# Optimization experiments

Hardware: AMD Instinct MI355X
Metric: run time of the kernel (lower is better)

The kernel has to match this reference:

```python
import jax, jax.numpy as jnp
import numpy as np
from jax import lax

B = 32
ITERS = 100
ALPHA = 0.3  # keras LeakyReLU default alpha
BN_SCALE = np.float32(1.0 / np.sqrt(1.0 + 1e-3))  # inference BN, default moving stats (mean 0, var 1)


def _make_psf_mat():
    # Gaussian PSF mapping 5184 fine (72x72) code positions -> 81 coarse (9x9) pixels, mat shape (5184, 81)
    sigma = (150.0 / 100.0) * 9.0 / 64.0
    coarse = np.arange(9) + 0.5
    fine = (np.arange(72) + 0.5) * 9.0 / 72.0
    g = np.exp(-(fine[:, None] - coarse[None, :]) ** 2 / (2.0 * sigma ** 2))  # (72, 9)
    mat = np.einsum('ia,jb->ijab', g, g).reshape(5184, 81)
    mat = mat / np.linalg.norm(mat, ord=2)  # spectral-normalize so FISTA (mu=1) is stable
    return mat.astype(np.float32)


def leaky(x):
    return jnp.where(x >= 0, x, ALPHA * x)


def conv(x, k, strides=(1, 1)):
    return lax.conv_general_dilated(x, k, strides, 'SAME',
                                    dimension_numbers=('NHWC', 'HWIO', 'NHWC'))


def _forward(inp, mat, w1_k, w1_b, x1_k, x1_b, c51_k, c51_b, c15_k, c15_b,
             c55_k, c55_b, x2_k, x2_b, y17_k, y17_b, y71_k, y71_b, yc_k, yc_b,
             d1_k, d2_k, h1_w, h1_b, h2_w, h2_b, h3_w, h3_b):
    b = inp.shape[0]
    # w branch
    w = leaky(conv(inp, w1_k) + w1_b)  # (B,9,9,1)
    # z branch -> lambda parameter
    z = inp * BN_SCALE
    z = leaky(conv(z, d1_k, strides=(3, 3)) * BN_SCALE)  # (B,3,3,12), downsample: conv no-bias + BN + LeakyReLU
    z = leaky(conv(z, d2_k, strides=(3, 3)) * BN_SCALE)  # (B,1,1,24)
    z = z.reshape(b, -1)
    z = z @ h1_w + h1_b
    z = z @ h2_w + h2_b
    z = z @ h3_w + h3_b  # (B,1)
    param = 0.1 * jax.nn.sigmoid(z)  # (B,1)
    # x branch: normalize (max of |x| over axis 1 only, as in source)
    x = inp / (0.001 + jnp.max(jnp.abs(inp), axis=1, keepdims=True))
    x = leaky(conv(x, x1_k) + x1_b)  # (B,9,9,3)
    # --- CompressedSensing: 100-iter FISTA, vectorized over batch and 3 channels ---
    im = x.reshape(b, 81, 3).transpose(0, 2, 1)  # (B,3,81) row-major flatten per channel
    lam = (param * 0.1)[:, :, None]  # (B,1,1), mu = 1.0

    def step(carry, _):
        y_tmp, y_last, t = carry
        resid = im - jnp.einsum('bcn,nk->bck', y_tmp, mat)      # (B,3,81)  = im - mat^T y
        re = jnp.einsum('bck,nk->bcn', resid, mat)              # (B,3,5184) = mat (im - mat^T y)
        wv = y_tmp + re
        y_new = jax.nn.relu(wv - lam) - jax.nn.relu(-wv - lam)  # soft threshold
        t_n = (1.0 + jnp.sqrt(1.0 + 4.0 * t * t)) / 2.0
        y_next = y_new + (t - 1.0) / t_n * (y_new - y_last)
        return (y_next, y_new, t_n), None

    init = (jnp.zeros((b, 3, 5184), jnp.float32),
            jnp.zeros((b, 3, 5184), jnp.float32),
            jnp.float32(1.0))
    (_, y_new, _), _ = lax.scan(step, init, None, length=ITERS)
    cs_out = y_new.transpose(0, 2, 1).reshape(b, 72, 72, 3)  # stack channels last then reshape
    x = conv(cs_out, c51_k, strides=(2, 2)) + c51_b   # (B,36,36,16), no activation
    x = conv(x, c15_k, strides=(2, 2)) + c15_b        # (B,18,18,32)
    x = conv(x, c55_k, strides=(2, 2)) + c55_b        # (B,9,9,64)
    x = leaky(conv(x, x2_k) + x2_b)                   # (B,9,9,8)
    # y branch
    y1 = conv(inp, y17_k) + y17_b                     # (B,9,9,32)
    y2 = conv(inp, y71_k) + y71_b                     # (B,9,9,32)
    y = leaky(conv(jnp.concatenate([y1, y2], axis=-1), yc_k) + yc_b)  # (B,9,9,32)
    out = jnp.concatenate([w, x, y], axis=-1)         # (B,9,9,41)
    return out, cs_out


def setup_inputs() -> dict:
    key = jax.random.key(0)
    ks = jax.random.split(key, 20)
    rn = lambda k, s, sc=0.1: sc * jax.random.normal(k, s, dtype=jnp.float32)
    x1_k = jnp.clip(1.0 + 0.3 * jax.random.normal(ks[1], (1, 1, 3, 3)), 0.0, None).astype(jnp.float32)
    return {
        'inp': jax.random.normal(ks[0], (B, 9, 9, 3), dtype=jnp.float32),
        'mat': jnp.asarray(_make_psf_mat()),
        'w1_k': rn(ks[2], (1, 1, 3, 1)), 'w1_b': jnp.zeros((1,), jnp.float32),
        'x1_k': x1_k, 'x1_b': jnp.zeros((3,), jnp.float32),
        'c51_k': rn(ks[3], (5, 1, 3, 16)), 'c51_b': jnp.zeros((16,), jnp.float32),
        'c15_k': rn(ks[4], (1, 5, 16, 32)), 'c15_b': jnp.zeros((32,), jnp.float32),
        'c55_k': rn(ks[5], (5, 5, 32, 64)), 'c55_b': jnp.zeros((64,), jnp.float32),
        'x2_k': rn(ks[6], (1, 1, 64, 8)), 'x2_b': jnp.zeros((8,), jnp.float32),
        'y17_k': rn(ks[7], (1, 7, 3, 32)), 'y17_b': jnp.zeros((32,), jnp.float32),
        'y71_k': rn(ks[8], (7, 1, 3, 32)), 'y71_b': jnp.zeros((32,), jnp.float32),
        'yc_k': rn(ks[9], (1, 1, 64, 32)), 'yc_b': jnp.zeros((32,), jnp.float32),
        'd1_k': rn(ks[10], (5, 5, 3, 12)), 'd2_k': rn(ks[11], (5, 5, 12, 24)),
        'h1_w': rn(ks[12], (24, 24), 0.2), 'h1_b': jnp.zeros((24,), jnp.float32),
        'h2_w': rn(ks[13], (24, 12), 0.2), 'h2_b': jnp.zeros((12,), jnp.float32),
        'h3_w': rn(ks[14], (12, 1), 0.2), 'h3_b': jnp.zeros((1,), jnp.float32),
    }


def reference(inp, mat, w1_k, w1_b, x1_k, x1_b, c51_k, c51_b, c15_k, c15_b,
              c55_k, c55_b, x2_k, x2_b, y17_k, y17_b, y71_k, y71_b, yc_k, yc_b,
              d1_k, d2_k, h1_w, h1_b, h2_w, h2_b, h3_w, h3_b):
    return _forward(inp, mat, w1_k, w1_b, x1_k, x1_b, c51_k, c51_b, c15_k, c15_b,
                    c55_k, c55_b, x2_k, x2_b, y17_k, y17_b, y71_k, y71_b, yc_k, yc_b,
                    d1_k, d2_k, h1_w, h1_b, h2_w, h2_b, h3_w, h3_b)
```

## Files before the change

### kernel.cpp

```cpp
#include <hip/hip_runtime.h>
#include <math.h>

#define LEAKY(x) ((x) >= 0.f ? (x) : 0.3f*(x))

#define G_OFF   0
#define IM_OFF  648
#define LAM_OFF 8424
#define WB_OFF  8456
#define YBR_OFF 11048
#define X2_OFF  757544

#define OUT0 106272

__global__ __launch_bounds__(256) void prep_kernel(
    const float* __restrict__ inp, const float* __restrict__ mat,
    const float* __restrict__ w1_k, const float* __restrict__ w1_b,
    const float* __restrict__ x1_k, const float* __restrict__ x1_b,
    const float* __restrict__ y17_k, const float* __restrict__ y17_b,
    const float* __restrict__ y71_k, const float* __restrict__ y71_b,
    const float* __restrict__ yc_k, const float* __restrict__ yc_b,
    const float* __restrict__ d1_k, const float* __restrict__ d2_k,
    const float* __restrict__ h1_w, const float* __restrict__ h1_b,
    const float* __restrict__ h2_w, const float* __restrict__ h2_b,
    const float* __restrict__ h3_w, const float* __restrict__ h3_b,
    float* __restrict__ ws)
{
    int t = threadIdx.x;
    if (blockIdx.x == 0) {
        float rs = rsqrtf(mat[0]);
        for (int u = t; u < 648; u += 256) {
            int i = u / 9, a = u % 9;
            ws[G_OFF + u] = mat[(size_t)(i*72)*81 + a*9] * rs;
        }
        return;
    }
    int b = blockIdx.x - 1;
    __shared__ float sin_[243];
    __shared__ float cm[27];
    __shared__ float cat[5184];
    __shared__ float z1[108];
    __shared__ float z2[24];
    __shared__ float v1[24];
    __shared__ float v2[12];

    const float BN  = 1.0f / sqrtf(1.001f);
    const float BN2 = BN * BN;

    for (int u = t; u < 243; u += 256) sin_[u] = inp[b*243 + u];
    __syncthreads();

    if (t < 81) {
        float s = w1_b[0];
        for (int i = 0; i < 3; ++i) s += sin_[t*3+i] * w1_k[i];
        ws[WB_OFF + b*81 + t] = LEAKY(s);
    } else if (t < 108) {
        int u = t - 81;
        float m = 0.f;
        for (int r = 0; r < 9; ++r) m = fmaxf(m, fabsf(sin_[r*27 + u]));
        cm[u] = 0.001f + m;
    }
    if (t >= 128 && t < 236) {
        int u = t - 128;
        int o = u % 12, ox = (u/12) % 3, oy = u/36;
        float s = 0.f;
        for (int kh = 0; kh < 5; ++kh) {
            int iy = oy*3 - 1 + kh;
            if (iy < 0 || iy > 8) continue;
            for (int kw = 0; kw < 5; ++kw) {
                int ix = ox*3 - 1 + kw;
                if (ix < 0 || ix > 8) continue;
                for (int i = 0; i < 3; ++i)
                    s += sin_[(iy*9+ix)*3 + i] * d1_k[((kh*5+kw)*3 + i)*12 + o];
            }
        }
        z1[u] = LEAKY(BN2 * s);
    }
    __syncthreads();

    if (t < 243) {
        int o = t / 81, p = t % 81;
        int c = p % 9;
        float s = x1_b[o];
        for (int i = 0; i < 3; ++i)
            s += (sin_[p*3+i] / cm[c*3+i]) * x1_k[i*3 + o];
        ws[IM_OFF + (b*3 + o)*81 + p] = LEAKY(s);
    }
    __syncthreads();

    if (t < 24) {
        float s = 0.f;
        for (int kh = 1; kh < 4; ++kh)
            for (int kw = 1; kw < 4; ++kw)
                for (int i = 0; i < 12; ++i)
                    s += z1[((kh-1)*3 + (kw-1))*12 + i] * d2_k[((kh*5+kw)*12 + i)*24 + t];
        z2[t] = LEAKY(BN * s);
    }
    __syncthreads();
    if (t < 24) {
        float s = h1_b[t];
        for (int i = 0; i < 24; ++i) s += z2[i] * h1_w[i*24 + t];
        v1[t] = s;
    }
    __syncthreads();
    if (t < 12) {
        float s = h2_b[t];
        for (int i = 0; i < 24; ++i) s += v1[i] * h2_w[i*12 + t];
        v2[t] = s;
    }
    __syncthreads();
    if (t == 0) {
        float s = h3_b[0];
        for (int i = 0; i < 12; ++i) s += v2[i] * h3_w[i];
        ws[LAM_OFF + b] = 0.01f / (1.f + expf(-s));
    }

    for (int u = t; u < 5184; u += 256) {
        int pos = u / 64, i = u % 64;
        int r = pos / 9, c = pos % 9;
        float s;
        if (i < 32) {
            s = y17_b[i];
            for (int kw = 0; kw < 7; ++kw) {
                int cc = c - 3 + kw;
                if (cc < 0 || cc > 8) continue;
                for (int ii = 0; ii < 3; ++ii)
                    s += sin_[(r*9+cc)*3 + ii] * y17_k[(kw*3+ii)*32 + i];
            }
        } else {
            int i2 = i - 32;
            s = y71_b[i2];
            for (int kh = 0; kh < 7; ++kh) {
                int rr = r - 3 + kh;
                if (rr < 0 || rr > 8) continue;
                for (int ii = 0; ii < 3; ++ii)
                    s += sin_[(rr*9+c)*3 + ii] * y71_k[(kh*3+ii)*32 + i2];
            }
        }
        cat[pos*64 + i] = s;
    }
    __syncthreads();
    for (int u = t; u < 2592; u += 256) {
        int pos = u / 32, o = u % 32;
        float s = yc_b[o];
        for (int i = 0; i < 64; ++i) s += cat[pos*64 + i] * yc_k[i*32 + o];
        ws[YBR_OFF + (b*81 + pos)*32 + o] = LEAKY(s);
    }
}


#define DPP_XOR1 0xB1
#define DPP_XOR2 0x4E
#define DPP_HM   0x141
#define DPP_ROR8 0x128

template<int CTRL>
__device__ __forceinline__ float dppadd(float v) {
    return v + __int_as_float(__builtin_amdgcn_update_dpp(
        0, __float_as_int(v), CTRL, 0xF, 0xF, true));
}

#define STEPMID(s,sm,sp) { \
    float re = gm*q##sm + g0*q##s + gp*q##sp; \
    float wv = Yv##s + re; \
    float cl = fminf(fmaxf(wv, -lam), lam); \
    float yn = wv - cl; \
    float yx = yn + cmom*(yn - Yl##s); \
    Yl##s = yn; Yv##s = yx; \
    u##sm += yx*gm; u##s += yx*g0; u##sp += yx*gp; }
#define STEP0 { \
    float re = g0*q0 + gp*q1; \
    float wv = Yv0 + re; \
    float cl = fminf(fmaxf(wv, -lam), lam); \
    float yn = wv - cl; \
    float yx = yn + cmom*(yn - Yl0); \
    Yl0 = yn; Yv0 = yx; \
    u0 += yx*g0; u1 += yx*gp; }
#define STEP8 { \
    float re = gm*q7 + g0*q8; \
    float wv = Yv8 + re; \
    float cl = fminf(fmaxf(wv, -lam), lam); \
    float yn = wv - cl; \
    float yx = yn + cmom*(yn - Yl8); \
    Yl8 = yn; Yv8 = yx; \
    u7 += yx*gm; u8 += yx*g0; }

#define TSP(a) { float v = u##a; \
    v = dppadd<DPP_XOR1>(v); v = dppadd<DPP_XOR2>(v); v = dppadd<DPP_HM>(v); \
    float vA = v*Gjg, vB = v*Gj8; \
    spA_##a = dppadd<DPP_ROR8>(vA); spB_##a = dppadd<DPP_ROR8>(vB); }

#define QT3(a) float q##a = cmc*rm_##a + c0c*r0_##a + cpc*rp_##a;

#define OUTW(s) cs_out[(size_t)(b*5184 + (8*s+gg)*72 + j)*3 + ch] = Yl##s;

__global__ __launch_bounds__(576, 3) void fista_kernel(
    const float* __restrict__ ws, float* __restrict__ cs_out)
{
    __shared__ __align__(16) float SPm[36*108];
    __shared__ __align__(16) float Rm[108];

    int t = threadIdx.x;
    int b = blockIdx.x / 3, ch = blockIdx.x % 3;
    const float* g = ws + G_OFF;
    float lam = ws[LAM_OFF + b];

    int j = t >> 3, gg = t & 7;
    int l = t & 63;
    int w = t >> 6;
    int rr = j & 7;

    float gm = g[(gg + 8)*9 + 0];
    float g0 = g[gg*9 + 0];
    float gp = g[gg*9 + 1];

    float cmc = (w > 0) ? g[(rr + 8)*9 + 0] : 0.f;
    float c0c = g[rr*9 + 0];
    float cpc = (w < 8) ? g[rr*9 + 1] : 0.f;
    int bmr = (w > 0) ? w - 1 : 0;
    int bpr = (w < 8) ? w + 1 : 8;

    float Gjg = g[j*9 + gg];
    float Gj8 = g[j*9 + 8];

    int ab = t >> 2, pp = t & 3;
    int aa = ab / 9, bb = ab % 9;
    float im_ab = (t < 324) ? ws[IM_OFF + (b*3 + ch)*81 + ab] : 0.f;

    if (t < 81) {
        Rm[(t % 9)*12 + (t / 9)] = ws[IM_OFF + (b*3 + ch)*81 + t];
    }

    float Yv0=0,Yv1=0,Yv2=0,Yv3=0,Yv4=0,Yv5=0,Yv6=0,Yv7=0,Yv8=0;
    float Yl0=0,Yl1=0,Yl2=0,Yl3=0,Yl4=0,Yl5=0,Yl6=0,Yl7=0,Yl8=0;
    float tk = 1.f;
    __syncthreads();

    for (int it = 0; it < 100; ++it) {
        float tn = 0.5f*(1.f + sqrtf(1.f + 4.f*tk*tk));
        float cmom = (tk - 1.f) / tn;
        tk = tn;

        float4 mv0 = *(const float4*)(Rm + bmr*12);
        float4 mv1 = *(const float4*)(Rm + bmr*12 + 4);
        float  mv2 = Rm[bmr*12 + 8];
        float rm_0=mv0.x, rm_1=mv0.y, rm_2=mv0.z, rm_3=mv0.w,
              rm_4=mv1.x, rm_5=mv1.y, rm_6=mv1.z, rm_7=mv1.w, rm_8=mv2;
        float4 zv0 = *(const float4*)(Rm + w*12);
        float4 zv1 = *(const float4*)(Rm + w*12 + 4);
        float  zv2 = Rm[w*12 + 8];
        float r0_0=zv0.x, r0_1=zv0.y, r0_2=zv0.z, r0_3=zv0.w,
              r0_4=zv1.x, r0_5=zv1.y, r0_6=zv1.z, r0_7=zv1.w, r0_8=zv2;
        float4 pv0 = *(const float4*)(Rm + bpr*12);
        float4 pv1 = *(const float4*)(Rm + bpr*12 + 4);
        float  pv2 = Rm[bpr*12 + 8];
        float rp_0=pv0.x, rp_1=pv0.y, rp_2=pv0.z, rp_3=pv0.w,
              rp_4=pv1.x, rp_5=pv1.y, rp_6=pv1.z, rp_7=pv1.w, rp_8=pv2;
        QT3(0) QT3(1) QT3(2) QT3(3) QT3(4) QT3(5) QT3(6) QT3(7) QT3(8)

        float u0=0,u1=0,u2=0,u3=0,u4=0,u5=0,u6=0,u7=0,u8=0;
        STEP0
        STEPMID(1,0,2) STEPMID(2,1,3) STEPMID(3,2,4) STEPMID(4,3,5)
        STEPMID(5,4,6) STEPMID(6,5,7) STEPMID(7,6,8)
        STEP8
        if (it == 99) break;

        float spA_0,spA_1,spA_2,spA_3,spA_4,spA_5,spA_6,spA_7,spA_8;
        float spB_0,spB_1,spB_2,spB_3,spB_4,spB_5,spB_6,spB_7,spB_8;
        TSP(0) TSP(1) TSP(2) TSP(3) TSP(4) TSP(5) TSP(6) TSP(7) TSP(8)

        int setb = ((t >> 6)*4 + (l >> 4))*108;
        if ((l & 8) == 0) {
            float* d = &SPm[setb + gg*12];
            ((float4*)d)[0] = make_float4(spA_0,spA_1,spA_2,spA_3);
            ((float4*)d)[1] = make_float4(spA_4,spA_5,spA_6,spA_7);
            d[8] = spA_8;
            if (gg == 0) {
                float* d2 = &SPm[setb + 96];
                ((float4*)d2)[0] = make_float4(spB_0,spB_1,spB_2,spB_3);
                ((float4*)d2)[1] = make_float4(spB_4,spB_5,spB_6,spB_7);
                d2[8] = spB_8;
            }
        }
        __syncthreads();

        if (t < 324) {
            float s = SPm[(bb*4 + pp)*108 + bb*12 + aa];
            if (bb > 0) s += SPm[((bb-1)*4 + pp)*108 + bb*12 + aa];
            if (bb < 8) s += SPm[((bb+1)*4 + pp)*108 + bb*12 + aa];
            s = dppadd<DPP_XOR1>(s);
            s = dppadd<DPP_XOR2>(s);
            if (pp == 0) Rm[bb*12 + aa] = im_ab - s;
        }
        __syncthreads();
    }

    OUTW(0) OUTW(1) OUTW(2) OUTW(3) OUTW(4) OUTW(5) OUTW(6) OUTW(7) OUTW(8)
}

__global__ __launch_bounds__(256) void c51c15_kernel(
    const float* __restrict__ cs, const float* __restrict__ k51,
    const float* __restrict__ b51, const float* __restrict__ k15,
    const float* __restrict__ b15, float* __restrict__ x2out)
{
    __shared__ float x1s[36*16];
    int t = threadIdx.x;
    int b = blockIdx.x / 18, oy = blockIdx.x % 18;

    for (int u = t; u < 36*16; u += 256) {
        int o = u & 15, ox = u >> 4;
        float s = b51[o];
        int ix = ox*2;
        for (int kh = 0; kh < 5; ++kh) {
            int iy = oy*4 - 1 + kh;
            if (iy < 0 || iy >= 72) continue;
            const float* p = cs + ((size_t)(b*72 + iy)*72 + ix)*3;
            const float* kk = k51 + kh*48 + o;
            s += p[0]*kk[0] + p[1]*kk[16] + p[2]*kk[32];
        }
        x1s[u] = s;
    }
    __syncthreads();

    for (int u = t; u < 18*32; u += 256) {
        int o = u & 31, ox = u >> 5;
        float s = b15[o];
        for (int kw = 0; kw < 5; ++kw) {
            int ix = ox*2 - 1 + kw;
            if (ix < 0 || ix >= 36) continue;
            const float* p = x1s + ix*16;
            const float* kk = k15 + kw*512 + o;
            for (int i = 0; i < 16; ++i) s += p[i]*kk[i*32];
        }
        x2out[((size_t)(b*18 + oy)*18 + ox)*32 + o] = s;
    }
}

__global__ __launch_bounds__(256) void c55out_kernel(
    const float* __restrict__ x2g, const float* __restrict__ k55,
    const float* __restrict__ b55, const float* __restrict__ ws,
    const float* __restrict__ x2_k, const float* __restrict__ x2_b,
    float* __restrict__ out)
{
    __shared__ float x3s[4][64];
    int t = threadIdx.x;
    int lp = t >> 6;
    int o  = t & 63;
    int pg = blockIdx.x*4 + lp;
    int b  = pg / 81, rc = pg % 81;
    int r  = rc / 9,  c  = rc % 9;

    {
        float s = b55[o];
        for (int kh = 0; kh < 5; ++kh) {
            int iy = r*2 - 1 + kh;
            if (iy < 0 || iy >= 18) continue;
            for (int kw = 0; kw < 5; ++kw) {
                int ix = c*2 - 1 + kw;
                if (ix < 0 || ix >= 18) continue;
                const float* p = x2g + ((size_t)(b*18 + iy)*18 + ix)*32;
                const float* kk = k55 + (kh*5+kw)*2048 + o;
                for (int i = 0; i < 32; ++i) s += p[i]*kk[i*64];
            }
        }
        x3s[lp][o] = s;
    }
    __syncthreads();

    if (t < 4*41) {
        int lp2 = t / 41, q = t % 41;
        int pg2 = blockIdx.x*4 + lp2;
        int b2  = pg2 / 81, rc2 = pg2 % 81;
        float val;
        if (q == 0) {
            val = ws[WB_OFF + b2*81 + rc2];
        } else if (q <= 8) {
            int o2 = q - 1;
            float s = x2_b[o2];
            for (int i = 0; i < 64; ++i) s += x3s[lp2][i]*x2_k[i*8 + o2];
            val = LEAKY(s);
        } else {
            val = ws[YBR_OFF + (size_t)(b2*81 + rc2)*32 + (q - 9)];
        }
        out[(size_t)pg2*41 + q] = val;
    }
}

extern "C" void kernel_launch(void* const* d_in, const int* in_sizes, int n_in,
                              void* d_out, int out_size, void* d_ws, size_t ws_size,
                              hipStream_t stream) {
    const float* inp   = (const float*)d_in[0];
    const float* mat   = (const float*)d_in[1];
    const float* w1_k  = (const float*)d_in[2];
    const float* w1_b  = (const float*)d_in[3];
    const float* x1_k  = (const float*)d_in[4];
    const float* x1_b  = (const float*)d_in[5];
    const float* c51_k = (const float*)d_in[6];
    const float* c51_b = (const float*)d_in[7];
    const float* c15_k = (const float*)d_in[8];
    const float* c15_b = (const float*)d_in[9];
    const float* c55_k = (const float*)d_in[10];
    const float* c55_b = (const float*)d_in[11];
    const float* x2_k  = (const float*)d_in[12];
    const float* x2_b  = (const float*)d_in[13];
    const float* y17_k = (const float*)d_in[14];
    const float* y17_b = (const float*)d_in[15];
    const float* y71_k = (const float*)d_in[16];
    const float* y71_b = (const float*)d_in[17];
    const float* yc_k  = (const float*)d_in[18];
    const float* yc_b  = (const float*)d_in[19];
    const float* d1_k  = (const float*)d_in[20];
    const float* d2_k  = (const float*)d_in[21];
    const float* h1_w  = (const float*)d_in[22];
    const float* h1_b  = (const float*)d_in[23];
    const float* h2_w  = (const float*)d_in[24];
    const float* h2_b  = (const float*)d_in[25];
    const float* h3_w  = (const float*)d_in[26];
    const float* h3_b  = (const float*)d_in[27];

    float* ws  = (float*)d_ws;
    float* out = (float*)d_out;
    float* cs  = out + OUT0;

    hipLaunchKernelGGL(prep_kernel, dim3(33), dim3(256), 0, stream,
        inp, mat, w1_k, w1_b, x1_k, x1_b, y17_k, y17_b, y71_k, y71_b,
        yc_k, yc_b, d1_k, d2_k, h1_w, h1_b, h2_w, h2_b, h3_w, h3_b, ws);
    hipLaunchKernelGGL(fista_kernel, dim3(96), dim3(576), 0, stream, ws, cs);
    hipLaunchKernelGGL(c51c15_kernel, dim3(576), dim3(256), 0, stream,
        cs, c51_k, c51_b, c15_k, c15_b, ws + X2_OFF);
    hipLaunchKernelGGL(c55out_kernel, dim3(648), dim3(256), 0, stream,
        ws + X2_OFF, c55_k, c55_b, ws, x2_k, x2_b, out);
}
```

Before: 346.7 us.

## Double-buffer partial sums and give each wavefront a private residual copy

```diff
diff --git a/kernel.cpp b/kernel.cpp
--- a/kernel.cpp
+++ b/kernel.cpp
@@ -152,6 +152,8 @@
 #define DPP_XOR2 0x4E
 #define DPP_HM   0x141
 #define DPP_ROR8 0x128
+
+#define SPHALF 3888
 
 template<int CTRL>
 __device__ __forceinline__ float dppadd(float v) {
@@ -196,8 +198,8 @@
 __global__ __launch_bounds__(576, 3) void fista_kernel(
     const float* __restrict__ ws, float* __restrict__ cs_out)
 {
-    __shared__ __align__(16) float SPm[36*108];
-    __shared__ __align__(16) float Rm[108];
+    __shared__ __align__(16) float SPm[2*SPHALF];
+    __shared__ __align__(16) float Rpriv[9*36];
 
     int t = threadIdx.x;
     int b = blockIdx.x / 3, ch = blockIdx.x % 3;
@@ -216,43 +218,48 @@
     float cmc = (w > 0) ? g[(rr + 8)*9 + 0] : 0.f;
     float c0c = g[rr*9 + 0];
     float cpc = (w < 8) ? g[rr*9 + 1] : 0.f;
-    int bmr = (w > 0) ? w - 1 : 0;
-    int bpr = (w < 8) ? w + 1 : 8;
 
     float Gjg = g[j*9 + gg];
     float Gj8 = g[j*9 + 8];
 
-    int ab = t >> 2, pp = t & 3;
-    int aa = ab / 9, bb = ab % 9;
-    float im_ab = (t < 324) ? ws[IM_OFF + (b*3 + ch)*81 + ab] : 0.f;
-
-    if (t < 81) {
-        Rm[(t % 9)*12 + (t / 9)] = ws[IM_OFF + (b*3 + ch)*81 + t];
-    }
+    int r3 = l / 18, rrem = l % 18, ra = rrem >> 1, rh = rrem & 1;
+    bool ract = (l < 54);
+    int rb = w - 1 + r3;
+    bool rbval = ract && (rb >= 0) && (rb <= 8);
+    int rbc = rb < 0 ? 0 : (rb > 8 ? 8 : rb);
+    int slotc = rbc*12 + ra;
+    int wmv = rbc > 0 ? rbc - 1 : 0;
+    int wpv = rbc < 8 ? rbc + 1 : 8;
+    float mmsk = (rbc > 0) ? 1.f : 0.f;
+    float mpsk = (rbc < 8) ? 1.f : 0.f;
+    int p0 = rh*2;
+    float im_reg = rbval ? ws[IM_OFF + (b*3 + ch)*81 + ra*9 + rb] : 0.f;
+
+    if (ract && rh == 0) Rpriv[w*36 + r3*12 + ra] = rbval ? im_reg : 0.f;
 
     float Yv0=0,Yv1=0,Yv2=0,Yv3=0,Yv4=0,Yv5=0,Yv6=0,Yv7=0,Yv8=0;
     float Yl0=0,Yl1=0,Yl2=0,Yl3=0,Yl4=0,Yl5=0,Yl6=0,Yl7=0,Yl8=0;
     float tk = 1.f;
-    __syncthreads();
 
     for (int it = 0; it < 100; ++it) {
         float tn = 0.5f*(1.f + sqrtf(1.f + 4.f*tk*tk));
         float cmom = (tk - 1.f) / tn;
         tk = tn;
 
-        float4 mv0 = *(const float4*)(Rm + bmr*12);
-        float4 mv1 = *(const float4*)(Rm + bmr*12 + 4);
-        float  mv2 = Rm[bmr*12 + 8];
+        const float* Rw = Rpriv + w*36;
+        float4 mv0 = *(const float4*)(Rw);
+        float4 mv1 = *(const float4*)(Rw + 4);
+        float  mv2 = Rw[8];
         float rm_0=mv0.x, rm_1=mv0.y, rm_2=mv0.z, rm_3=mv0.w,
               rm_4=mv1.x, rm_5=mv1.y, rm_6=mv1.z, rm_7=mv1.w, rm_8=mv2;
-        float4 zv0 = *(const float4*)(Rm + w*12);
-        float4 zv1 = *(const float4*)(Rm + w*12 + 4);
-        float  zv2 = Rm[w*12 + 8];
+        float4 zv0 = *(const float4*)(Rw + 12);
+        float4 zv1 = *(const float4*)(Rw + 16);
+        float  zv2 = Rw[20];
         float r0_0=zv0.x, r0_1=zv0.y, r0_2=zv0.z, r0_3=zv0.w,
               r0_4=zv1.x, r0_5=zv1.y, r0_6=zv1.z, r0_7=zv1.w, r0_8=zv2;
-        float4 pv0 = *(const float4*)(Rm + bpr*12);
-        float4 pv1 = *(const float4*)(Rm + bpr*12 + 4);
-        float  pv2 = Rm[bpr*12 + 8];
+        float4 pv0 = *(const float4*)(Rw + 24);
+        float4 pv1 = *(const float4*)(Rw + 28);
+        float  pv2 = Rw[32];
         float rp_0=pv0.x, rp_1=pv0.y, rp_2=pv0.z, rp_3=pv0.w,
               rp_4=pv1.x, rp_5=pv1.y, rp_6=pv1.z, rp_7=pv1.w, rp_8=pv2;
         QT3(0) QT3(1) QT3(2) QT3(3) QT3(4) QT3(5) QT3(6) QT3(7) QT3(8)
@@ -268,14 +275,15 @@
         float spB_0,spB_1,spB_2,spB_3,spB_4,spB_5,spB_6,spB_7,spB_8;
         TSP(0) TSP(1) TSP(2) TSP(3) TSP(4) TSP(5) TSP(6) TSP(7) TSP(8)
 
-        int setb = ((t >> 6)*4 + (l >> 4))*108;
+        float* SP = SPm + (it & 1)*SPHALF;
+        int setb = (w*4 + (l >> 4))*108;
         if ((l & 8) == 0) {
-            float* d = &SPm[setb + gg*12];
+            float* d = SP + setb + gg*12;
             ((float4*)d)[0] = make_float4(spA_0,spA_1,spA_2,spA_3);
             ((float4*)d)[1] = make_float4(spA_4,spA_5,spA_6,spA_7);
             d[8] = spA_8;
             if (gg == 0) {
-                float* d2 = &SPm[setb + 96];
+                float* d2 = SP + setb + 96;
                 ((float4*)d2)[0] = make_float4(spB_0,spB_1,spB_2,spB_3);
                 ((float4*)d2)[1] = make_float4(spB_4,spB_5,spB_6,spB_7);
                 d2[8] = spB_8;
@@ -283,15 +291,15 @@
         }
         __syncthreads();
 
-        if (t < 324) {
-            float s = SPm[(bb*4 + pp)*108 + bb*12 + aa];
-            if (bb > 0) s += SPm[((bb-1)*4 + pp)*108 + bb*12 + aa];
-            if (bb < 8) s += SPm[((bb+1)*4 + pp)*108 + bb*12 + aa];
+        if (ract) {
+            const float* S = SPm + (it & 1)*SPHALF;
+            float s = S[(rbc*4 + p0)*108 + slotc] + S[(rbc*4 + p0+1)*108 + slotc]
+               + mmsk*(S[(wmv*4 + p0)*108 + slotc] + S[(wmv*4 + p0+1)*108 + slotc])
+               + mpsk*(S[(wpv*4 + p0)*108 + slotc] + S[(wpv*4 + p0+1)*108 + slotc]);
             s = dppadd<DPP_XOR1>(s);
-            s = dppadd<DPP_XOR2>(s);
-            if (pp == 0) Rm[bb*12 + aa] = im_ab - s;
-        }
-        __syncthreads();
+            if (rh == 0)
+                Rpriv[w*36 + r3*12 + ra] = rbval ? (im_reg - s) : 0.f;
+        }
     }
 
     OUTW(0) OUTW(1) OUTW(2) OUTW(3) OUTW(4) OUTW(5) OUTW(6) OUTW(7) OUTW(8)
```

After: 338.7 us. 1.02x faster.
